# Kernel optimization log

Hardware: AMD Instinct MI355X
Metric: run time of the kernel (lower is better)

Reference implementation:

```python
import jax, jax.numpy as jnp
import numpy as np

N_NODES = 100000
N_EDGES = 3200000
DIM_IN = 256
DIM_OUT = 256


def setup_inputs() -> dict:
    key = jax.random.key(0)
    k1, k2, k3, k4, k5 = jax.random.split(key, 5)
    x = jax.random.normal(k1, (N_NODES, DIM_IN), dtype=jnp.float32)
    adj_rows = jax.random.randint(k2, (N_EDGES,), 0, N_NODES, dtype=jnp.int64)
    adj_cols = jax.random.randint(k3, (N_EDGES,), 0, N_NODES, dtype=jnp.int64)
    adj_vals = jax.random.uniform(k4, (N_EDGES,), dtype=jnp.float32)
    # torch Linear weight: [dim_out, dim_in]
    W = jax.random.normal(k5, (DIM_OUT, DIM_IN), dtype=jnp.float32) * (1.0 / np.sqrt(DIM_IN))
    return {"x": x, "adj_rows": adj_rows, "adj_cols": adj_cols, "adj_vals": adj_vals, "W": W}


def reference(x, adj_rows, adj_cols, adj_vals, W):
    # h = Linear(x) with no bias -> x @ W.T  : [N, dim_out]
    h = jnp.einsum('nd,od->no', x, W)
    # sparse.mm(adjacency, h): out[r] = sum_{edges e with row r} val[e] * h[col[e]]
    msgs = adj_vals[:, None] * h[adj_cols]            # [E, dim_out]
    out = jax.ops.segment_sum(msgs, adj_rows, num_segments=N_NODES)
    return out
```

## Files before the change

kernel.cpp:

```cpp
#include <hip/hip_runtime.h>
#include <hip/hip_bf16.h>

#define DIM 256
#define GRP 4
#define CAP8 56
#define OVF_CAP 65536
#define NSCAT 2048

typedef short s16x8 __attribute__((ext_vector_type(8)));
typedef float f32x4 __attribute__((ext_vector_type(4)));

__device__ inline unsigned short f32_bf16_rne(float f) {
    unsigned u = __float_as_uint(f);
    u += 0x7FFFu + ((u >> 16) & 1u);
    return (unsigned short)(u >> 16);
}
__device__ inline float bf16_f32(unsigned short h) {
    return __uint_as_float(((unsigned)h) << 16);
}
__device__ inline float4 bf16x4_f32(uint2 p) {
    float4 r;
    r.x = __uint_as_float(p.x << 16);
    r.y = __uint_as_float(p.x & 0xFFFF0000u);
    r.z = __uint_as_float(p.y << 16);
    r.w = __uint_as_float(p.y & 0xFFFF0000u);
    return r;
}

__global__ __launch_bounds__(256) void prep_w(const float* __restrict__ W,
                                              unsigned short* __restrict__ Wh) {
    int i = blockIdx.x * 256 + threadIdx.x;
    Wh[i] = f32_bf16_rne(W[i]);
}

__device__ __forceinline__ void gemm_body(const float* __restrict__ X,
                                          const unsigned short* __restrict__ Wh,
                                          unsigned short* __restrict__ H, int N, int gb,
                                          unsigned short* xh, unsigned short* xl) {
    const int tid = threadIdx.x;
    const int lane = tid & 63;
    const int wv = tid >> 6;
    const int bm = gb * 64;

    const int srow = tid & 63;
    const int schunk = tid >> 6;
    const int grow = bm + srow;
    const bool rowok = grow < N;
    const float* xsrc = X + (size_t)grow * DIM + schunk * 8;
    const int swch = srow * 4 + (schunk ^ ((srow >> 1) & 3));

    const int frow = lane & 15;
    const int fch = lane >> 4;

    f32x4 acc[4][4] = {};

    for (int k0 = 0; k0 < DIM; k0 += 32) {
        float v[8];
        if (rowok) {
            float4 a = *(const float4*)(xsrc + k0);
            float4 b = *(const float4*)(xsrc + k0 + 4);
            v[0] = a.x; v[1] = a.y; v[2] = a.z; v[3] = a.w;
            v[4] = b.x; v[5] = b.y; v[6] = b.z; v[7] = b.w;
        } else {
#pragma unroll
            for (int e = 0; e < 8; ++e) v[e] = 0.f;
        }
        unsigned hh[8], ll[8];
#pragma unroll
        for (int e = 0; e < 8; ++e) {
            unsigned short hu = f32_bf16_rne(v[e]);
            hh[e] = hu;
            ll[e] = f32_bf16_rne(v[e] - bf16_f32(hu));
        }
        uint4 hv = make_uint4(hh[0] | (hh[1] << 16), hh[2] | (hh[3] << 16),
                              hh[4] | (hh[5] << 16), hh[6] | (hh[7] << 16));
        uint4 lv = make_uint4(ll[0] | (ll[1] << 16), ll[2] | (ll[3] << 16),
                              ll[4] | (ll[5] << 16), ll[6] | (ll[7] << 16));
        ((uint4*)xh)[swch] = hv;
        ((uint4*)xl)[swch] = lv;
        __syncthreads();

        s16x8 ah[4], al[4], bh[4];
#pragma unroll
        for (int i = 0; i < 4; ++i) {
            int row = i * 16 + frow;
            int rch = row * 4 + (fch ^ ((row >> 1) & 3));
            ah[i] = __builtin_bit_cast(s16x8, ((const uint4*)xh)[rch]);
            al[i] = __builtin_bit_cast(s16x8, ((const uint4*)xl)[rch]);
        }
#pragma unroll
        for (int j = 0; j < 4; ++j) {
            size_t off = (size_t)(wv * 64 + j * 16 + frow) * DIM + k0 + fch * 8;
            bh[j] = __builtin_bit_cast(s16x8, *(const uint4*)(Wh + off));
        }
#pragma unroll
        for (int i = 0; i < 4; ++i)
#pragma unroll
            for (int j = 0; j < 4; ++j) {
                acc[i][j] = __builtin_amdgcn_mfma_f32_16x16x32_bf16(ah[i], bh[j], acc[i][j], 0, 0, 0);
                acc[i][j] = __builtin_amdgcn_mfma_f32_16x16x32_bf16(al[i], bh[j], acc[i][j], 0, 0, 0);
            }
        __syncthreads();
    }

#pragma unroll
    for (int i = 0; i < 4; ++i)
#pragma unroll
        for (int r = 0; r < 4; ++r) {
            int row = bm + i * 16 + fch * 4 + r;
            if (row < N) {
#pragma unroll
                for (int j = 0; j < 4; ++j)
                    H[(size_t)row * DIM + wv * 64 + j * 16 + frow] = f32_bf16_rne(acc[i][j][r]);
            }
        }
}

__device__ __forceinline__ void scatter_body(const int* __restrict__ rows,
                                             const int* __restrict__ cols,
                                             const float* __restrict__ vals,
                                             int* __restrict__ cur,
                                             unsigned long long* __restrict__ buckets,
                                             uint4* __restrict__ ovf,
                                             int* __restrict__ ovf_cnt,
                                             int nE, int B4, int sb) {
    unsigned xcd;
    asm volatile("s_getreg_b32 %0, hwreg(HW_REG_XCC_ID)" : "=s"(xcd));
    xcd &= 7;

    int i = sb * 256 + threadIdx.x;
    int st = NSCAT * 256;
    for (int e = i; e < nE; e += st) {
        int r = rows[e];
        unsigned c = (unsigned)cols[e];
        unsigned vb = __float_as_uint(vals[e]);
        int cell = (int)xcd * B4 + (r >> 2);
        int p = atomicAdd(&cur[cell], 1);
        if (p < CAP8) {
            unsigned lo = c | ((unsigned)(r & 3) << 17);
            buckets[(size_t)cell * CAP8 + p] = (unsigned long long)lo | ((unsigned long long)vb << 32);
        } else {
            int q = atomicAdd(ovf_cnt, 1);
            if (q < OVF_CAP) ovf[q] = make_uint4((unsigned)r, c, vb, 0u);
        }
    }
}

__global__ __launch_bounds__(256) void fused_sg(const float* __restrict__ X,
                                                const unsigned short* __restrict__ Wh,
                                                unsigned short* __restrict__ H,
                                                const int* __restrict__ rows,
                                                const int* __restrict__ cols,
                                                const float* __restrict__ vals,
                                                int* __restrict__ cur,
                                                unsigned long long* __restrict__ buckets,
                                                uint4* __restrict__ ovf,
                                                int* __restrict__ ovf_cnt,
                                                int N, int nE, int B4) {
    __shared__ __align__(16) unsigned short xh[64 * 32];
    __shared__ __align__(16) unsigned short xl[64 * 32];

    if (blockIdx.x < NSCAT) {
        scatter_body(rows, cols, vals, cur, buckets, ovf, ovf_cnt, nE, B4, blockIdx.x);
    } else {
        gemm_body(X, Wh, H, N, blockIdx.x - NSCAT, xh, xl);
    }
}

__global__ __launch_bounds__(256) void gemm_mfma(const float* __restrict__ X,
                                                 const unsigned short* __restrict__ Wh,
                                                 unsigned short* __restrict__ H, int N) {
    __shared__ __align__(16) unsigned short xh[64 * 32];
    __shared__ __align__(16) unsigned short xl[64 * 32];
    gemm_body(X, Wh, H, N, blockIdx.x, xh, xl);
}

__global__ __launch_bounds__(256) void bucket_agg4(const unsigned short* __restrict__ hb,
                                                   const unsigned long long* __restrict__ buckets,
                                                   const int* __restrict__ cur,
                                                   float* __restrict__ out, int N, int B4) {
    const int lane = threadIdx.x & 63;
    const int g = (blockIdx.x * 256 + threadIdx.x) >> 6;
    if (g >= B4) return;

    f32x4 a0 = {0,0,0,0}, a1 = {0,0,0,0}, a2 = {0,0,0,0}, a3 = {0,0,0,0};

#define ACCUM(e, gth)                                                        \
    {                                                                        \
        float vv = __uint_as_float((unsigned)((e) >> 32));                   \
        int idx = (int)(((unsigned)(e) >> 17) & 3u);                         \
        float4 f = bf16x4_f32(gth);                                          \
        f32x4 d = {vv * f.x, vv * f.y, vv * f.z, vv * f.w};                  \
        switch (idx) {                                                       \
            case 0: a0 += d; break;  case 1: a1 += d; break;                 \
            case 2: a2 += d; break;  default: a3 += d; break;                \
        }                                                                    \
    }

    for (int x = 0; x < 8; ++x) {
        const int cell = x * B4 + g;
        const int cnt = min(cur[cell], CAP8);
        const unsigned long long* p = buckets + (size_t)cell * CAP8;

        int j = 0;
        for (; j + 8 <= cnt; j += 8) {
            unsigned long long e0 = __builtin_nontemporal_load(p + j);
            unsigned long long e1 = __builtin_nontemporal_load(p + j + 1);
            unsigned long long e2 = __builtin_nontemporal_load(p + j + 2);
            unsigned long long e3 = __builtin_nontemporal_load(p + j + 3);
            unsigned long long e4 = __builtin_nontemporal_load(p + j + 4);
            unsigned long long e5 = __builtin_nontemporal_load(p + j + 5);
            unsigned long long e6 = __builtin_nontemporal_load(p + j + 6);
            unsigned long long e7 = __builtin_nontemporal_load(p + j + 7);
            uint2 g0 = *(const uint2*)(hb + (size_t)((unsigned)e0 & 0x1FFFFu) * DIM + lane * 4);
            uint2 g1 = *(const uint2*)(hb + (size_t)((unsigned)e1 & 0x1FFFFu) * DIM + lane * 4);
            uint2 g2 = *(const uint2*)(hb + (size_t)((unsigned)e2 & 0x1FFFFu) * DIM + lane * 4);
            uint2 g3 = *(const uint2*)(hb + (size_t)((unsigned)e3 & 0x1FFFFu) * DIM + lane * 4);
            uint2 g4 = *(const uint2*)(hb + (size_t)((unsigned)e4 & 0x1FFFFu) * DIM + lane * 4);
            uint2 g5 = *(const uint2*)(hb + (size_t)((unsigned)e5 & 0x1FFFFu) * DIM + lane * 4);
            uint2 g6 = *(const uint2*)(hb + (size_t)((unsigned)e6 & 0x1FFFFu) * DIM + lane * 4);
            uint2 g7 = *(const uint2*)(hb + (size_t)((unsigned)e7 & 0x1FFFFu) * DIM + lane * 4);
            ACCUM(e0, g0) ACCUM(e1, g1) ACCUM(e2, g2) ACCUM(e3, g3)
            ACCUM(e4, g4) ACCUM(e5, g5) ACCUM(e6, g6) ACCUM(e7, g7)
        }
        for (; j < cnt; ++j) {
            unsigned long long e = __builtin_nontemporal_load(p + j);
            uint2 gv = *(const uint2*)(hb + (size_t)((unsigned)e & 0x1FFFFu) * DIM + lane * 4);
            ACCUM(e, gv)
        }
    }
#undef ACCUM

    const int r0 = g * GRP;
#define STORE_ROW(i, acc) \
    { int r = r0 + (i); if (r < N) __builtin_nontemporal_store(acc, (f32x4*)(out + (size_t)r * DIM + lane * 4)); }
    STORE_ROW(0, a0) STORE_ROW(1, a1) STORE_ROW(2, a2) STORE_ROW(3, a3)
#undef STORE_ROW
}

__global__ __launch_bounds__(256) void ovf_fix(const unsigned short* __restrict__ hb,
                                               const uint4* __restrict__ ovf,
                                               const int* __restrict__ ovf_cnt,
                                               float* __restrict__ out) {
    const int n = min(*ovf_cnt, OVF_CAP);
    const int lane = threadIdx.x & 63;
    const int w = (blockIdx.x * 256 + threadIdx.x) >> 6;
    const int nw = gridDim.x * 4;
    for (int e = w; e < n; e += nw) {
        uint4 t = ovf[e];
        float vv = __uint_as_float(t.z);
        float4 f = bf16x4_f32(*(const uint2*)(hb + (size_t)t.y * DIM + lane * 4));
        float* op = out + (size_t)t.x * DIM + lane * 4;
        atomicAdd(op + 0, vv * f.x);
        atomicAdd(op + 1, vv * f.y);
        atomicAdd(op + 2, vv * f.z);
        atomicAdd(op + 3, vv * f.w);
    }
}

__global__ __launch_bounds__(256) void edge_scatter(const unsigned short* __restrict__ hb,
                                                    const int* __restrict__ rows,
                                                    const int* __restrict__ cols,
                                                    const float* __restrict__ vals,
                                                    float* __restrict__ out, int nE) {
    const int lane = threadIdx.x & 63;
    const int wave = (blockIdx.x * blockDim.x + threadIdx.x) >> 6;
    const int nWaves = (gridDim.x * blockDim.x) >> 6;
    for (int e = wave; e < nE; e += nWaves) {
        const int r = rows[e];
        const int c = cols[e];
        const float v = vals[e];
        float4 f = bf16x4_f32(*(const uint2*)(hb + (size_t)c * DIM + lane * 4));
        float* op = out + (size_t)r * DIM + lane * 4;
        atomicAdd(op + 0, v * f.x);
        atomicAdd(op + 1, v * f.y);
        atomicAdd(op + 2, v * f.z);
        atomicAdd(op + 3, v * f.w);
    }
}

extern "C" void kernel_launch(void* const* d_in, const int* in_sizes, int n_in,
                              void* d_out, int out_size, void* d_ws, size_t ws_size,
                              hipStream_t stream) {
    const float* x    = (const float*)d_in[0];
    const int*   rows = (const int*)d_in[1];
    const int*   cols = (const int*)d_in[2];
    const float* vals = (const float*)d_in[3];
    const float* W    = (const float*)d_in[4];

    float* out = (float*)d_out;
    const int N  = in_sizes[0] / DIM;
    const int nE = in_sizes[1];
    const int B4 = (N + GRP - 1) / GRP;
    const int cells = 8 * B4;

    auto align256 = [](size_t v) { return (v + 255) & ~(size_t)255; };
    char* ws = (char*)d_ws;

    size_t off_wh   = 0;
    size_t off_h    = align256(off_wh + (size_t)DIM * DIM * 2);
    size_t off_cur  = align256(off_h + (size_t)N * DIM * 2);
    size_t off_ovf  = align256(off_cur + (size_t)(cells + 64) * 4);
    size_t off_bkt  = align256(off_ovf + (size_t)OVF_CAP * 16);
    size_t total    = off_bkt + (size_t)cells * CAP8 * 8;

    unsigned short* Wh = (unsigned short*)(ws + off_wh);
    unsigned short* h  = (unsigned short*)(ws + off_h);

    const bool packOK = (N <= (1 << 17));

    prep_w<<<DIM * DIM / 256, 256, 0, stream>>>(W, Wh);

    if (ws_size >= total && packOK) {
        int*   cur     = (int*)(ws + off_cur);
        int*   ovf_cnt = cur + cells;
        uint4* ovf     = (uint4*)(ws + off_ovf);
        unsigned long long* bkt = (unsigned long long*)(ws + off_bkt);

        hipMemsetAsync(cur, 0, (size_t)(cells + 64) * 4, stream);

        const int nGemm = (N + 63) / 64;
        fused_sg<<<NSCAT + nGemm, 256, 0, stream>>>(x, Wh, h, rows, cols, vals,
                                                    cur, bkt, ovf, ovf_cnt, N, nE, B4);

        bucket_agg4<<<(B4 + 3) / 4, 256, 0, stream>>>(h, bkt, cur, out, N, B4);
        ovf_fix<<<32, 256, 0, stream>>>(h, ovf, ovf_cnt, out);
    } else {
        gemm_mfma<<<(N + 63) / 64, 256, 0, stream>>>(x, Wh, h, N);
        hipMemsetAsync(out, 0, (size_t)out_size * sizeof(float), stream);
        edge_scatter<<<2048, 256, 0, stream>>>(h, rows, cols, vals, out, nE);
    }
}
```

Before: 491.6 us.

## Interleave scatter and GEMM blocks in fused kernel, add nontemporal loads

```diff
diff --git a/kernel.cpp b/kernel.cpp
--- a/kernel.cpp
+++ b/kernel.cpp
@@ -5,7 +5,6 @@
 #define GRP 4
 #define CAP8 56
 #define OVF_CAP 65536
-#define NSCAT 2048
 
 typedef short s16x8 __attribute__((ext_vector_type(8)));
 typedef float f32x4 __attribute__((ext_vector_type(4)));
@@ -57,10 +56,10 @@
     for (int k0 = 0; k0 < DIM; k0 += 32) {
         float v[8];
         if (rowok) {
-            float4 a = *(const float4*)(xsrc + k0);
-            float4 b = *(const float4*)(xsrc + k0 + 4);
-            v[0] = a.x; v[1] = a.y; v[2] = a.z; v[3] = a.w;
-            v[4] = b.x; v[5] = b.y; v[6] = b.z; v[7] = b.w;
+            f32x4 a = __builtin_nontemporal_load((const f32x4*)(xsrc + k0));
+            f32x4 b = __builtin_nontemporal_load((const f32x4*)(xsrc + k0 + 4));
+            v[0] = a[0]; v[1] = a[1]; v[2] = a[2]; v[3] = a[3];
+            v[4] = b[0]; v[5] = b[1]; v[6] = b[2]; v[7] = b[3];
         } else {
 #pragma unroll
             for (int e = 0; e < 8; ++e) v[e] = 0.f;
@@ -123,17 +122,17 @@
                                              unsigned long long* __restrict__ buckets,
                                              uint4* __restrict__ ovf,
                                              int* __restrict__ ovf_cnt,
-                                             int nE, int B4, int sb) {
+                                             int nE, int B4, int sb, int nScat) {
     unsigned xcd;
     asm volatile("s_getreg_b32 %0, hwreg(HW_REG_XCC_ID)" : "=s"(xcd));
     xcd &= 7;
 
     int i = sb * 256 + threadIdx.x;
-    int st = NSCAT * 256;
+    int st = nScat * 256;
     for (int e = i; e < nE; e += st) {
-        int r = rows[e];
-        unsigned c = (unsigned)cols[e];
-        unsigned vb = __float_as_uint(vals[e]);
+        int r = __builtin_nontemporal_load(rows + e);
+        unsigned c = (unsigned)__builtin_nontemporal_load(cols + e);
+        unsigned vb = __builtin_bit_cast(unsigned, __builtin_nontemporal_load(vals + e));
         int cell = (int)xcd * B4 + (r >> 2);
         int p = atomicAdd(&cur[cell], 1);
         if (p < CAP8) {
@@ -156,14 +155,16 @@
                                                 unsigned long long* __restrict__ buckets,
                                                 uint4* __restrict__ ovf,
                                                 int* __restrict__ ovf_cnt,
-                                                int N, int nE, int B4) {
+                                                int N, int nE, int B4, int nScat) {
     __shared__ __align__(16) unsigned short xh[64 * 32];
     __shared__ __align__(16) unsigned short xl[64 * 32];
 
-    if (blockIdx.x < NSCAT) {
-        scatter_body(rows, cols, vals, cur, buckets, ovf, ovf_cnt, nE, B4, blockIdx.x);
+    const int bid = blockIdx.x;
+    if (bid % 7 == 3) {
+        scatter_body(rows, cols, vals, cur, buckets, ovf, ovf_cnt, nE, B4, bid / 7, nScat);
     } else {
-        gemm_body(X, Wh, H, N, blockIdx.x - NSCAT, xh, xl);
+        int gidx = bid - (bid + 3) / 7;
+        gemm_body(X, Wh, H, N, gidx, xh, xl);
     }
 }
 
@@ -320,8 +321,12 @@
         hipMemsetAsync(cur, 0, (size_t)(cells + 64) * 4, stream);
 
         const int nGemm = (N + 63) / 64;
-        fused_sg<<<NSCAT + nGemm, 256, 0, stream>>>(x, Wh, h, rows, cols, vals,
-                                                    cur, bkt, ovf, ovf_cnt, N, nE, B4);
+        int nScat = 0;
+        for (int it = 0; it < 8; ++it) nScat = (nGemm + nScat + 3) / 7;
+        const int grid = nGemm + nScat;
+
+        fused_sg<<<grid, 256, 0, stream>>>(x, Wh, h, rows, cols, vals,
+                                           cur, bkt, ovf, ovf_cnt, N, nE, B4, nScat);
 
         bucket_agg4<<<(B4 + 3) / 4, 256, 0, stream>>>(h, bkt, cur, out, N, B4);
         ovf_fix<<<32, 256, 0, stream>>>(h, ovf, ovf_cnt, out);
```

Result: slower. 528.2 us (+7.4%).
